# Optimization experiments

Measured on AMD Instinct MI355X. Metric: run time of the kernel, lower is better.

## Reference

```python
import jax, jax.numpy as jnp
import numpy as np

T, B, D, H = 512, 256, 64, 128  # timesteps, num_envs, obs_dim, lstm hidden


def setup_inputs() -> dict:
    key = jax.random.key(0)
    ks = jax.random.split(key, 8)
    x = jax.random.normal(ks[0], (T, B, D), dtype=jnp.float32)
    done = (jax.random.uniform(ks[1], (T, B)) < 0.02).astype(jnp.float32)
    h0 = 0.01 * jax.random.normal(ks[2], (B, H), dtype=jnp.float32)
    c0 = 0.01 * jax.random.normal(ks[3], (B, H), dtype=jnp.float32)
    W_ih = jax.random.normal(ks[4], (4 * H, D), dtype=jnp.float32) / np.sqrt(D)
    W_hh = jax.random.normal(ks[5], (4 * H, H), dtype=jnp.float32) / np.sqrt(H)
    b_ih = jnp.zeros((4 * H,), dtype=jnp.float32)
    b_hh = jnp.zeros((4 * H,), dtype=jnp.float32)
    W_hid = jax.random.normal(ks[6], (H, H), dtype=jnp.float32) * np.sqrt(2.0 / H)
    b_hid = jnp.zeros((H,), dtype=jnp.float32)
    return {"x": x, "done": done, "h0": h0, "c0": c0,
            "W_ih": W_ih, "b_ih": b_ih, "W_hh": W_hh, "b_hh": b_hh,
            "W_hid": W_hid, "b_hid": b_hid}


def reference(x, done, h0, c0, W_ih, b_ih, W_hh, b_hh, W_hid, b_hid):
    # Precompute input contribution to gates for all timesteps: [T, B, 4H]
    xg = jnp.einsum('tbd,gd->tbg', x, W_ih) + b_ih + b_hh

    def step(carry, inp):
        h, c = carry            # [B, H] each
        xg_t, d = inp           # [B, 4H], [B]
        mask = (1.0 - d)[:, None]
        h = h * mask            # reset state where episode ended
        c = c * mask
        gates = xg_t + h @ W_hh.T            # [B, 4H]
        i, f, g, o = jnp.split(gates, 4, axis=-1)  # PyTorch gate order i,f,g,o
        c = jax.nn.sigmoid(f) * c + jax.nn.sigmoid(i) * jnp.tanh(g)
        h = jax.nn.sigmoid(o) * jnp.tanh(c)
        return (h, c), h

    (_, _), hs = jax.lax.scan(step, (h0, c0), (xg, done))  # hs: [T, B, H]
    hidden = hs.reshape(-1, H) @ W_hid.T + b_hid           # [T*B, H]
    return hidden
```

## Files before the change

### kernel.cpp

```cpp
#include <hip/hip_runtime.h>

#define T_STEPS 512
#define B_ENV   256
#define D_IN    64
#define H_DIM   128
#define G4      512

typedef _Float16 h2v __attribute__((ext_vector_type(2)));
typedef _Float16 h8v __attribute__((ext_vector_type(8)));
typedef float    f4v __attribute__((ext_vector_type(4)));
typedef __fp16   g2  __attribute__((ext_vector_type(2)));
typedef __fp16   g8  __attribute__((ext_vector_type(8)));

__device__ __forceinline__ float dot2(h2v a, h2v b, float c) {
#if __has_builtin(__builtin_amdgcn_fdot2)
    return __builtin_amdgcn_fdot2(a, b, c, false);
#else
    return c + (float)a.x * (float)b.x + (float)a.y * (float)b.y;
#endif
}

__device__ __forceinline__ g2 pack16g(float a, float b) {
#if __has_builtin(__builtin_amdgcn_cvt_pkrtz)
    return __builtin_amdgcn_cvt_pkrtz(a, b);
#else
    g2 p; p.x = (__fp16)a; p.y = (__fp16)b; return p;
#endif
}
__device__ __forceinline__ h2v pack16(float a, float b) {
    union { g2 r; h2v h; } u; u.r = pack16g(a, b); return u.h;
}

__device__ __forceinline__ f4v mfma16(g8 a, g8 b, f4v c) {
    return __builtin_amdgcn_mfma_f32_16x16x32_f16(a, b, c, 0, 0, 0);
}

__device__ __forceinline__ float fast_rcp(float x) {
#if __has_builtin(__builtin_amdgcn_rcpf)
    return __builtin_amdgcn_rcpf(x);
#else
    return 1.0f / x;
#endif
}
__device__ __forceinline__ float sigm(float x)   { return fast_rcp(1.0f + __expf(-x)); }
__device__ __forceinline__ float tanh_f(float x) { float e = __expf(2.0f * x); return 1.0f - 2.0f * fast_rcp(e + 1.0f); }

template <int CTRL>
__device__ __forceinline__ float dpp_mov(float v) {
    int s = __builtin_amdgcn_update_dpp(
        0, __builtin_bit_cast(int, v), CTRL, 0xF, 0xF, true);
    return __builtin_bit_cast(float, s);
}
__device__ __forceinline__ float quad_allreduce(float v) {
    v += dpp_mov<0xB1>(v);
    v += dpp_mov<0x4E>(v);
    return v;
}

__device__ __forceinline__ void sync_lds() {
    asm volatile("s_waitcnt lgkmcnt(0)" ::: "memory");
    __builtin_amdgcn_s_barrier();
    asm volatile("" ::: "memory");
}

__global__ __launch_bounds__(256)
void ppo_xg(const float* __restrict__ x,
            const float* __restrict__ W_ih,
            const float* __restrict__ b_ih,
            const float* __restrict__ b_hh,
            unsigned short* __restrict__ xg)
{
    const int tid  = threadIdx.x;
    const int lane = tid & 63;
    const int w    = tid >> 6;
    const int rml  = lane & 15;
    const int colg = lane >> 4;

    __shared__ h2v   wl[G4][36];
    __shared__ float bl[G4];

    #pragma unroll
    for (int i = 0; i < 32; ++i) {
        const int idx = tid + 256 * i;
        const int r = idx >> 4, cc = idx & 15;
        f4v v = *reinterpret_cast<const f4v*>(W_ih + (size_t)idx * 4);
        wl[r][2 * cc]     = pack16(v.x, v.y);
        wl[r][2 * cc + 1] = pack16(v.z, v.w);
    }
    bl[tid]       = b_ih[tid]       + b_hh[tid];
    bl[tid + 256] = b_ih[tid + 256] + b_hh[tid + 256];
    __syncthreads();

    const size_t row0 = (size_t)blockIdx.x * 64 + w * 16;

    g8 a[2];
    #pragma unroll
    for (int ks = 0; ks < 2; ++ks) {
        const float* p = x + (row0 + rml) * D_IN + ks * 32 + colg * 8;
        union { g2 q[4]; g8 v; } u;
        #pragma unroll
        for (int c = 0; c < 4; ++c) u.q[c] = pack16g(p[2 * c], p[2 * c + 1]);
        a[ks] = u.v;
    }

    #pragma unroll 4
    for (int ct = 0; ct < 32; ++ct) {
        const int col = ct * 16 + rml;
        const g8 b0 = *reinterpret_cast<const g8*>(&wl[col][colg * 4]);
        const g8 b1 = *reinterpret_cast<const g8*>(&wl[col][16 + colg * 4]);
        const float bb = bl[col];
        f4v acc = {bb, bb, bb, bb};
        acc = mfma16(a[0], b0, acc);
        acc = mfma16(a[1], b1, acc);
        #pragma unroll
        for (int reg = 0; reg < 4; ++reg) {
            const __fp16 hv = (__fp16)acc[reg];
            xg[(row0 + colg * 4 + reg) * G4 + ct * 16 + rml] =
                __builtin_bit_cast(unsigned short, hv);
        }
    }
}

__global__ __launch_bounds__(512, 1) __attribute__((amdgpu_waves_per_eu(2, 2)))
void ppo_lstm_scan_xg(const unsigned short* __restrict__ xg,
                      const float* __restrict__ done,
                      const float* __restrict__ h0,
                      const float* __restrict__ c0,
                      const float* __restrict__ W_hh,
                      float* __restrict__ hs)
{
    const int b   = blockIdx.x;
    const int tid = threadIdx.x;
    const int qq  = tid & 3;
    const int j   = tid >> 2;

    __shared__ alignas(16) h2v   h16[2][H_DIM / 2];
    __shared__ alignas(16) float smask[T_STEPS];

    h2v whh[64];
    #pragma unroll
    for (int g = 0; g < 4; ++g) {
        const float* wr = W_hh + (size_t)(g * H_DIM + j) * H_DIM + qq * 32;
        #pragma unroll
        for (int c = 0; c < 16; ++c)
            whh[g * 16 + c] = pack16(wr[2 * c], wr[2 * c + 1]);
    }
    const float m0 = (qq == 0) ? 1.f : 0.f;
    const float m1 = (qq == 1) ? 1.f : 0.f;
    const float m2 = (qq == 2) ? 1.f : 0.f;
    const float m3 = (qq == 3) ? 1.f : 0.f;
    float c_reg = c0[b * H_DIM + j];

    smask[tid] = 1.0f - done[(size_t)tid * B_ENV + b];
    if (tid < 64) {
        const float sm0 = 1.0f - done[b];
        const float* hp = h0 + b * H_DIM;
        h16[0][tid] = pack16(hp[2 * tid] * sm0, hp[2 * tid + 1] * sm0);
    }
    const size_t XSTR = (size_t)B_ENV * G4;
    const unsigned short* xgp = xg + (size_t)b * G4 + (qq * H_DIM + j);
    unsigned short xcur = xgp[0];
    float* hsp = hs + (size_t)b * H_DIM + j;
    __syncthreads();

    float dm = 1.0f - done[b];

    #pragma unroll 2
    for (int t = 0; t < T_STEPS - 1; ++t) {
        const int rb = t & 1, wb = rb ^ 1;

        const float xgf = (float)__builtin_bit_cast(__fp16, xcur);
        float s0 = xgf * m0, s1 = xgf * m1, s2 = xgf * m2, s3 = xgf * m3;

        xgp += XSTR;
        const unsigned short xnext = xgp[0];

        const h8v* hp8 = reinterpret_cast<const h8v*>(&h16[rb][qq * 16]);
        #pragma unroll
        for (int c4 = 0; c4 < 4; ++c4) {
            union { h8v v; h2v p[4]; } u;
            u.v = hp8[c4];
            #pragma unroll
            for (int pp = 0; pp < 4; ++pp) {
                s0 = dot2(whh[      c4 * 4 + pp], u.p[pp], s0);
                s1 = dot2(whh[16 +  c4 * 4 + pp], u.p[pp], s1);
                s2 = dot2(whh[32 +  c4 * 4 + pp], u.p[pp], s2);
                s3 = dot2(whh[48 +  c4 * 4 + pp], u.p[pp], s3);
            }
        }

        s0 = quad_allreduce(s0);
        s1 = quad_allreduce(s1);
        s2 = quad_allreduce(s2);
        s3 = quad_allreduce(s3);

        const float gi = sigm(s0);
        const float gf = sigm(s1);
        const float gg = tanh_f(s2);
        const float go = sigm(s3);

        const float cn = gf * (c_reg * dm) + gi * gg;
        c_reg = cn;
        const float hn = go * tanh_f(cn);

        const float smn = smask[t + 1];
        if (qq == 0) {
            reinterpret_cast<_Float16*>(h16[wb])[j] = (_Float16)(hn * smn);
            hsp[0] = hn;
        }
        hsp += (size_t)B_ENV * H_DIM;
        dm   = smn;
        xcur = xnext;
        sync_lds();
    }

    {
        const int rb = (T_STEPS - 1) & 1;
        const float xgf = (float)__builtin_bit_cast(__fp16, xcur);
        float s0 = xgf * m0, s1 = xgf * m1, s2 = xgf * m2, s3 = xgf * m3;
        const h8v* hp8 = reinterpret_cast<const h8v*>(&h16[rb][qq * 16]);
        #pragma unroll
        for (int c4 = 0; c4 < 4; ++c4) {
            union { h8v v; h2v p[4]; } u;
            u.v = hp8[c4];
            #pragma unroll
            for (int pp = 0; pp < 4; ++pp) {
                s0 = dot2(whh[      c4 * 4 + pp], u.p[pp], s0);
                s1 = dot2(whh[16 +  c4 * 4 + pp], u.p[pp], s1);
                s2 = dot2(whh[32 +  c4 * 4 + pp], u.p[pp], s2);
                s3 = dot2(whh[48 +  c4 * 4 + pp], u.p[pp], s3);
            }
        }
        s0 = quad_allreduce(s0);
        s1 = quad_allreduce(s1);
        s2 = quad_allreduce(s2);
        s3 = quad_allreduce(s3);
        const float gi = sigm(s0);
        const float gf = sigm(s1);
        const float gg = tanh_f(s2);
        const float go = sigm(s3);
        const float cn = gf * (c_reg * dm) + gi * gg;
        const float hn = go * tanh_f(cn);
        if (qq == 0) hsp[0] = hn;
    }
}

__global__ __launch_bounds__(512, 1) __attribute__((amdgpu_waves_per_eu(2, 2)))
void ppo_lstm_scan_fb(const float* __restrict__ x,
                      const float* __restrict__ done,
                      const float* __restrict__ h0,
                      const float* __restrict__ c0,
                      const float* __restrict__ W_ih,
                      const float* __restrict__ b_ih,
                      const float* __restrict__ W_hh,
                      const float* __restrict__ b_hh,
                      float* __restrict__ hs)
{
    const int b   = blockIdx.x;
    const int tid = threadIdx.x;
    const int qq  = tid & 3;
    const int j   = tid >> 2;

    __shared__ alignas(16) h2v   h16[2][H_DIM / 2];
    __shared__ alignas(16) float smask[T_STEPS];

    h2v whh[64];
    h2v wih[32];
    #pragma unroll
    for (int g = 0; g < 4; ++g) {
        const float* wr = W_hh + (size_t)(g * H_DIM + j) * H_DIM + qq * 32;
        #pragma unroll
        for (int c = 0; c < 16; ++c)
            whh[g * 16 + c] = pack16(wr[2 * c], wr[2 * c + 1]);
        const float* wr2 = W_ih + (size_t)(g * H_DIM + j) * D_IN + qq * 16;
        #pragma unroll
        for (int c = 0; c < 8; ++c)
            wih[g * 8 + c] = pack16(wr2[2 * c], wr2[2 * c + 1]);
    }
    const int   r_own    = qq * H_DIM + j;
    const float bias_own = b_ih[r_own] + b_hh[r_own];
    float       c_reg    = c0[b * H_DIM + j];

    smask[tid] = 1.0f - done[(size_t)tid * B_ENV + b];
    if (tid < 64) {
        const float sm0 = 1.0f - done[b];
        const float* hp = h0 + b * H_DIM;
        h16[0][tid] = pack16(hp[2 * tid] * sm0, hp[2 * tid + 1] * sm0);
    }
    f4v xr[4];
    {
        const float* xp = x + (size_t)b * D_IN + qq * 16;
        #pragma unroll
        for (int i = 0; i < 4; ++i)
            xr[i] = *reinterpret_cast<const f4v*>(xp + 4 * i);
    }
    __syncthreads();

    for (int t = 0; t < T_STEPS; ++t) {
        const int rb = t & 1, wb = rb ^ 1;

        h2v xh[8];
        #pragma unroll
        for (int i = 0; i < 4; ++i) {
            xh[2 * i]     = pack16(xr[i].x, xr[i].y);
            xh[2 * i + 1] = pack16(xr[i].z, xr[i].w);
        }
        {
            const int tn = (t + 1 < T_STEPS) ? (t + 1) : t;
            const float* xp = x + ((size_t)tn * B_ENV + b) * D_IN + qq * 16;
            #pragma unroll
            for (int i = 0; i < 4; ++i)
                xr[i] = *reinterpret_cast<const f4v*>(xp + 4 * i);
        }

        const h8v* hp8 = reinterpret_cast<const h8v*>(&h16[rb][qq * 16]);
        float s0 = 0.f, s1 = 0.f, s2 = 0.f, s3 = 0.f;
        #pragma unroll
        for (int c4 = 0; c4 < 4; ++c4) {
            union { h8v v; h2v p[4]; } u;
            u.v = hp8[c4];
            #pragma unroll
            for (int pp = 0; pp < 4; ++pp) {
                s0 = dot2(whh[      c4 * 4 + pp], u.p[pp], s0);
                s1 = dot2(whh[16 +  c4 * 4 + pp], u.p[pp], s1);
                s2 = dot2(whh[32 +  c4 * 4 + pp], u.p[pp], s2);
                s3 = dot2(whh[48 +  c4 * 4 + pp], u.p[pp], s3);
            }
        }
        #pragma unroll
        for (int c = 0; c < 8; ++c) {
            s0 = dot2(wih[     c], xh[c], s0);
            s1 = dot2(wih[ 8 + c], xh[c], s1);
            s2 = dot2(wih[16 + c], xh[c], s2);
            s3 = dot2(wih[24 + c], xh[c], s3);
        }

        s0 = quad_allreduce(s0);
        s1 = quad_allreduce(s1);
        s2 = quad_allreduce(s2);
        s3 = quad_allreduce(s3);

        const float s01 = (qq & 1) ? s1 : s0;
        const float s23 = (qq & 1) ? s3 : s2;
        const float gs  = ((qq & 2) ? s23 : s01) + bias_own;
        const float av  = (qq == 2) ? tanh_f(gs) : sigm(gs);
        const float ai  = dpp_mov<0x00>(av);
        const float af  = dpp_mov<0x55>(av);
        const float ag  = dpp_mov<0xAA>(av);
        const float ao  = dpp_mov<0xFF>(av);

        const float dm = smask[t];
        const float cn = af * (c_reg * dm) + ai * ag;
        c_reg = cn;
        const float hn = ao * tanh_f(cn);

        if (qq == 0) {
            const float smn = smask[(t + 1 < T_STEPS) ? (t + 1) : (T_STEPS - 1)];
            reinterpret_cast<_Float16*>(h16[wb])[j] = (_Float16)(hn * smn);
            hs[((size_t)t * B_ENV + b) * H_DIM + j] = hn;
        }
        sync_lds();
    }
}

#define PADK 68
__global__ __launch_bounds__(256)
void ppo_proj(const float* __restrict__ W_hid,
              const float* __restrict__ b_hid,
              float* __restrict__ out)
{
    __shared__ h2v wl[H_DIM][PADK];
    __shared__ h2v hl[H_DIM][PADK];
    const int tid = threadIdx.x;
    const int rg  = tid >> 4;
    const int cg  = tid & 15;

    const size_t r0 = (size_t)blockIdx.x * H_DIM;

    #pragma unroll
    for (int i = 0; i < 16; ++i) {
        const int idx = tid + 256 * i;
        const int r = idx >> 5, cc = idx & 31;
        f4v v = *reinterpret_cast<const f4v*>(W_hid + 4 * (size_t)idx);
        wl[r][2 * cc]     = pack16(v.x, v.y);
        wl[r][2 * cc + 1] = pack16(v.z, v.w);
    }
    #pragma unroll
    for (int i = 0; i < 16; ++i) {
        const int idx = tid + 256 * i;
        const int r = idx >> 5, cc = idx & 31;
        f4v v = *reinterpret_cast<const f4v*>(out + (r0 + r) * H_DIM + 4 * cc);
        hl[r][2 * cc]     = pack16(v.x, v.y);
        hl[r][2 * cc + 1] = pack16(v.z, v.w);
    }
    float bcol[8];
    #pragma unroll
    for (int jj = 0; jj < 8; ++jj) bcol[jj] = b_hid[cg + 16 * jj];
    __syncthreads();

    float acc[8][8];
    #pragma unroll
    for (int i = 0; i < 8; ++i)
        #pragma unroll
        for (int jj = 0; jj < 8; ++jj) acc[i][jj] = 0.f;

    for (int kq = 0; kq < 16; ++kq) {
        union { h8v v; h2v p[4]; } hv[8], wv[8];
        #pragma unroll
        for (int i = 0; i < 8; ++i)
            hv[i].v = *reinterpret_cast<const h8v*>(&hl[rg * 8 + i][4 * kq]);
        #pragma unroll
        for (int jj = 0; jj < 8; ++jj)
            wv[jj].v = *reinterpret_cast<const h8v*>(&wl[cg + 16 * jj][4 * kq]);
        #pragma unroll
        for (int i = 0; i < 8; ++i)
            #pragma unroll
            for (int jj = 0; jj < 8; ++jj) {
                acc[i][jj] = dot2(hv[i].p[0], wv[jj].p[0], acc[i][jj]);
                acc[i][jj] = dot2(hv[i].p[1], wv[jj].p[1], acc[i][jj]);
                acc[i][jj] = dot2(hv[i].p[2], wv[jj].p[2], acc[i][jj]);
                acc[i][jj] = dot2(hv[i].p[3], wv[jj].p[3], acc[i][jj]);
            }
    }

    #pragma unroll
    for (int i = 0; i < 8; ++i)
        #pragma unroll
        for (int jj = 0; jj < 8; ++jj)
            out[(r0 + rg * 8 + i) * H_DIM + cg + 16 * jj] = acc[i][jj] + bcol[jj];
}

extern "C" void kernel_launch(void* const* d_in, const int* in_sizes, int n_in,
                              void* d_out, int out_size, void* d_ws, size_t ws_size,
                              hipStream_t stream) {
    const float* x     = (const float*)d_in[0];
    const float* done  = (const float*)d_in[1];
    const float* h0    = (const float*)d_in[2];
    const float* c0    = (const float*)d_in[3];
    const float* W_ih  = (const float*)d_in[4];
    const float* b_ih  = (const float*)d_in[5];
    const float* W_hh  = (const float*)d_in[6];
    const float* b_hh  = (const float*)d_in[7];
    const float* W_hid = (const float*)d_in[8];
    const float* b_hid = (const float*)d_in[9];
    float* out = (float*)d_out;
    (void)n_in; (void)in_sizes; (void)out_size;

    const size_t xg_bytes = (size_t)T_STEPS * B_ENV * G4 * sizeof(unsigned short);
    if (ws_size >= xg_bytes) {
        unsigned short* xg = (unsigned short*)d_ws;
        hipLaunchKernelGGL(ppo_xg, dim3((T_STEPS * B_ENV) / 64), dim3(256), 0, stream,
                           x, W_ih, b_ih, b_hh, xg);
        hipLaunchKernelGGL(ppo_lstm_scan_xg, dim3(B_ENV), dim3(512), 0, stream,
                           xg, done, h0, c0, W_hh, out);
    } else {
        hipLaunchKernelGGL(ppo_lstm_scan_fb, dim3(B_ENV), dim3(512), 0, stream,
                           x, done, h0, c0, W_ih, b_ih, W_hh, b_hh, out);
    }
    hipLaunchKernelGGL(ppo_proj, dim3((T_STEPS * B_ENV) / H_DIM), dim3(256), 0, stream,
                       W_hid, b_hid, out);
}
```

Before: 399.9 us.

## Pack two envs per 1024-thread block and spread gate activations across the quad

The LSTM scan kernel now runs two environments per workgroup of 1024 threads, with separate LDS h buffers and masks for each half, which halves the block count and raises waves per EU. Before, every lane computed all four gate nonlinearities. Now each lane of a quad computes only its own gate's activation, adds xg afterward, and broadcasts the results with DPP moves, cutting transcendental work per step. The risks are register pressure from the 4-waves-per-EU target and a barrier that now spans both environments in the block.

```diff
diff --git a/kernel.cpp b/kernel.cpp
--- a/kernel.cpp
+++ b/kernel.cpp
@@ -121,21 +121,24 @@
     }
 }
 
-__global__ __launch_bounds__(512, 1) __attribute__((amdgpu_waves_per_eu(2, 2)))
-void ppo_lstm_scan_xg(const unsigned short* __restrict__ xg,
-                      const float* __restrict__ done,
-                      const float* __restrict__ h0,
-                      const float* __restrict__ c0,
-                      const float* __restrict__ W_hh,
-                      float* __restrict__ hs)
+__global__ __attribute__((amdgpu_flat_work_group_size(1024, 1024),
+                          amdgpu_waves_per_eu(4, 4)))
+void ppo_lstm_scan_xg2(const unsigned short* __restrict__ xg,
+                       const float* __restrict__ done,
+                       const float* __restrict__ h0,
+                       const float* __restrict__ c0,
+                       const float* __restrict__ W_hh,
+                       float* __restrict__ hs)
 {
-    const int b   = blockIdx.x;
-    const int tid = threadIdx.x;
-    const int qq  = tid & 3;
-    const int j   = tid >> 2;
-
-    __shared__ alignas(16) h2v   h16[2][H_DIM / 2];
-    __shared__ alignas(16) float smask[T_STEPS];
+    const int tid  = threadIdx.x;
+    const int half = tid >> 9;
+    const int l    = tid & 511;
+    const int b    = blockIdx.x * 2 + half;
+    const int qq   = l & 3;
+    const int j    = l >> 2;
+
+    __shared__ alignas(16) h2v   h16[2][2][H_DIM / 2];
+    __shared__ alignas(16) float smask[2][T_STEPS];
 
     h2v whh[64];
     #pragma unroll
@@ -145,17 +148,13 @@
         for (int c = 0; c < 16; ++c)
             whh[g * 16 + c] = pack16(wr[2 * c], wr[2 * c + 1]);
     }
-    const float m0 = (qq == 0) ? 1.f : 0.f;
-    const float m1 = (qq == 1) ? 1.f : 0.f;
-    const float m2 = (qq == 2) ? 1.f : 0.f;
-    const float m3 = (qq == 3) ? 1.f : 0.f;
     float c_reg = c0[b * H_DIM + j];
 
-    smask[tid] = 1.0f - done[(size_t)tid * B_ENV + b];
-    if (tid < 64) {
+    smask[half][l] = 1.0f - done[(size_t)l * B_ENV + b];
+    if (l < 64) {
         const float sm0 = 1.0f - done[b];
         const float* hp = h0 + b * H_DIM;
-        h16[0][tid] = pack16(hp[2 * tid] * sm0, hp[2 * tid + 1] * sm0);
+        h16[half][0][l] = pack16(hp[2 * l] * sm0, hp[2 * l + 1] * sm0);
     }
     const size_t XSTR = (size_t)B_ENV * G4;
     const unsigned short* xgp = xg + (size_t)b * G4 + (qq * H_DIM + j);
@@ -169,13 +168,11 @@
     for (int t = 0; t < T_STEPS - 1; ++t) {
         const int rb = t & 1, wb = rb ^ 1;
 
-        const float xgf = (float)__builtin_bit_cast(__fp16, xcur);
-        float s0 = xgf * m0, s1 = xgf * m1, s2 = xgf * m2, s3 = xgf * m3;
-
         xgp += XSTR;
         const unsigned short xnext = xgp[0];
 
-        const h8v* hp8 = reinterpret_cast<const h8v*>(&h16[rb][qq * 16]);
+        const h8v* hp8 = reinterpret_cast<const h8v*>(&h16[half][rb][qq * 16]);
+        float s0 = 0.f, s1 = 0.f, s2 = 0.f, s3 = 0.f;
         #pragma unroll
         for (int c4 = 0; c4 < 4; ++c4) {
             union { h8v v; h2v p[4]; } u;
@@ -194,18 +191,23 @@
         s2 = quad_allreduce(s2);
         s3 = quad_allreduce(s3);
 
-        const float gi = sigm(s0);
-        const float gf = sigm(s1);
-        const float gg = tanh_f(s2);
-        const float go = sigm(s3);
-
-        const float cn = gf * (c_reg * dm) + gi * gg;
+        const float xgf = (float)__builtin_bit_cast(__fp16, xcur);
+        const float s01 = (qq & 1) ? s1 : s0;
+        const float s23 = (qq & 1) ? s3 : s2;
+        const float gs  = ((qq & 2) ? s23 : s01) + xgf;
+        const float av  = (qq == 2) ? tanh_f(gs) : sigm(gs);
+        const float ai  = dpp_mov<0x00>(av);
+        const float af  = dpp_mov<0x55>(av);
+        const float ag  = dpp_mov<0xAA>(av);
+        const float ao  = dpp_mov<0xFF>(av);
+
+        const float cn = af * (c_reg * dm) + ai * ag;
         c_reg = cn;
-        const float hn = go * tanh_f(cn);
-
-        const float smn = smask[t + 1];
+        const float hn = ao * tanh_f(cn);
+
+        const float smn = smask[half][t + 1];
         if (qq == 0) {
-            reinterpret_cast<_Float16*>(h16[wb])[j] = (_Float16)(hn * smn);
+            reinterpret_cast<_Float16*>(h16[half][wb])[j] = (_Float16)(hn * smn);
             hsp[0] = hn;
         }
         hsp += (size_t)B_ENV * H_DIM;
@@ -216,9 +218,8 @@
 
     {
         const int rb = (T_STEPS - 1) & 1;
-        const float xgf = (float)__builtin_bit_cast(__fp16, xcur);
-        float s0 = xgf * m0, s1 = xgf * m1, s2 = xgf * m2, s3 = xgf * m3;
-        const h8v* hp8 = reinterpret_cast<const h8v*>(&h16[rb][qq * 16]);
+        const h8v* hp8 = reinterpret_cast<const h8v*>(&h16[half][rb][qq * 16]);
+        float s0 = 0.f, s1 = 0.f, s2 = 0.f, s3 = 0.f;
         #pragma unroll
         for (int c4 = 0; c4 < 4; ++c4) {
             union { h8v v; h2v p[4]; } u;
@@ -235,12 +236,17 @@
         s1 = quad_allreduce(s1);
         s2 = quad_allreduce(s2);
         s3 = quad_allreduce(s3);
-        const float gi = sigm(s0);
-        const float gf = sigm(s1);
-        const float gg = tanh_f(s2);
-        const float go = sigm(s3);
-        const float cn = gf * (c_reg * dm) + gi * gg;
-        const float hn = go * tanh_f(cn);
+        const float xgf = (float)__builtin_bit_cast(__fp16, xcur);
+        const float s01 = (qq & 1) ? s1 : s0;
+        const float s23 = (qq & 1) ? s3 : s2;
+        const float gs  = ((qq & 2) ? s23 : s01) + xgf;
+        const float av  = (qq == 2) ? tanh_f(gs) : sigm(gs);
+        const float ai  = dpp_mov<0x00>(av);
+        const float af  = dpp_mov<0x55>(av);
+        const float ag  = dpp_mov<0xAA>(av);
+        const float ao  = dpp_mov<0xFF>(av);
+        const float cn  = af * (c_reg * dm) + ai * ag;
+        const float hn  = ao * tanh_f(cn);
         if (qq == 0) hsp[0] = hn;
     }
 }
@@ -451,7 +457,7 @@
         unsigned short* xg = (unsigned short*)d_ws;
         hipLaunchKernelGGL(ppo_xg, dim3((T_STEPS * B_ENV) / 64), dim3(256), 0, stream,
                            x, W_ih, b_ih, b_hh, xg);
-        hipLaunchKernelGGL(ppo_lstm_scan_xg, dim3(B_ENV), dim3(512), 0, stream,
+        hipLaunchKernelGGL(ppo_lstm_scan_xg2, dim3(B_ENV / 2), dim3(1024), 0, stream,
                            xg, done, h0, c0, W_hh, out);
     } else {
         hipLaunchKernelGGL(ppo_lstm_scan_fb, dim3(B_ENV), dim3(512), 0, stream,
```

Measured after the change: 568.7 us. +42.2%, slower.
